# Kernel optimization log

Measured on AMD Instinct MI355X. Metric: run time of the kernel, lower is better.

The kernel has to match this reference:

```python
import jax, jax.numpy as jnp
import numpy as np

B, S, D, H, T_OUT = 256, 256, 64, 1024, 32  # batch, enc seq, input dim, hidden, decode steps


def setup_inputs() -> dict:
    key = jax.random.key(0)
    ks = jax.random.split(key, 15)
    p = lambda k, shape: jax.random.normal(k, shape, jnp.float32) * 0.05
    return {
        "X": jax.random.normal(ks[0], (B, S, D), jnp.float32),
        # encoder LSTM (2 layers); bias = b_ih + b_hh fused (same math)
        "enc_Wih0": p(ks[1], (4 * H, D)), "enc_Whh0": p(ks[2], (4 * H, H)), "enc_b0": p(ks[3], (4 * H,)),
        "enc_Wih1": p(ks[4], (4 * H, H)), "enc_Whh1": p(ks[5], (4 * H, H)), "enc_b1": p(ks[6], (4 * H,)),
        # decoder LSTM (2 layers, scalar input)
        "dec_Wih0": p(ks[7], (4 * H, 1)), "dec_Whh0": p(ks[8], (4 * H, H)), "dec_b0": p(ks[9], (4 * H,)),
        "dec_Wih1": p(ks[10], (4 * H, H)), "dec_Whh1": p(ks[11], (4 * H, H)), "dec_b1": p(ks[12], (4 * H,)),
        # output projection hidden -> 1
        "fc_W": p(ks[13], (1, H)), "fc_b": p(ks[14], (1,)),
    }


def _cell(x, h, c, Wih, Whh, b):
    # torch LSTM cell, gate order i, f, g, o
    gates = x @ Wih.T + h @ Whh.T + b  # [B, 4H]
    i, f, g, o = jnp.split(gates, 4, axis=-1)
    c = jax.nn.sigmoid(f) * c + jax.nn.sigmoid(i) * jnp.tanh(g)
    h = jax.nn.sigmoid(o) * jnp.tanh(c)
    return h, c


def reference(X, enc_Wih0, enc_Whh0, enc_b0, enc_Wih1, enc_Whh1, enc_b1,
              dec_Wih0, dec_Whh0, dec_b0, dec_Wih1, dec_Whh1, dec_b1,
              fc_W, fc_b):
    batch = X.shape[0]
    zeros = jnp.zeros((batch, H), X.dtype)

    def enc_layer(Wih, Whh, b, xs):  # xs: [S, B, Din]
        def step(carry, x_t):
            h, c = carry
            h, c = _cell(x_t, h, c, Wih, Whh, b)
            return (h, c), h
        (h, c), hs = jax.lax.scan(step, (zeros, zeros), xs)
        return hs, h, c

    xs = jnp.swapaxes(X, 0, 1)  # time-major [S, B, D]
    hs0, h0, c0 = enc_layer(enc_Wih0, enc_Whh0, enc_b0, xs)
    _, h1, c1 = enc_layer(enc_Wih1, enc_Whh1, enc_b1, hs0)

    inp0 = jnp.zeros((batch, 1), X.dtype)

    def dec_step(carry, _):
        dh0, dc0, dh1, dc1, inp = carry
        dh0, dc0 = _cell(inp, dh0, dc0, dec_Wih0, dec_Whh0, dec_b0)
        dh1, dc1 = _cell(dh0, dh1, dc1, dec_Wih1, dec_Whh1, dec_b1)
        pred = dh1 @ fc_W.T + fc_b  # [B, 1]; dropout is identity at inference
        return (dh0, dc0, dh1, dc1, pred), pred

    _, preds = jax.lax.scan(dec_step, (h0, c0, h1, c1, inp0), None, length=T_OUT)
    return jnp.transpose(preds, (1, 0, 2))  # [B, T_OUT, 1]
```

## Files before the change

### kernel.cpp

```cpp
#include <hip/hip_runtime.h>

#define B_ 256
#define S_ 256
#define D_ 64
#define H_ 1024
#define G4 4096
#define TOUT 32

typedef unsigned short u16;
typedef __attribute__((ext_vector_type(8))) short short8;
typedef __attribute__((ext_vector_type(4))) float float4v;

__device__ __forceinline__ float bf2f(u16 b) {
  return __uint_as_float(((unsigned int)b) << 16);
}
__device__ __forceinline__ u16 f2bf(float f) {
  unsigned int u = __float_as_uint(f);
  unsigned int r = (u + 0x7fffu + ((u >> 16) & 1u)) >> 16;
  return (u16)r;
}
__device__ __forceinline__ unsigned pack2(float a, float b) {
  return (unsigned)f2bf(a) | ((unsigned)f2bf(b) << 16);
}
__device__ __forceinline__ float sigm(float x) {
  return 1.f / (1.f + __expf(-x));
}
__device__ __forceinline__ float tanh_(float x) {
  float xc = fminf(fmaxf(x, -15.f), 15.f);
  float e = __expf(2.f * xc);
  return (e - 1.f) / (e + 1.f);
}

__global__ __launch_bounds__(256) void cvt_kernel(const float* __restrict__ src,
                                                  u16* __restrict__ dst, int n) {
  for (int i = blockIdx.x * blockDim.x + threadIdx.x; i < n;
       i += gridDim.x * blockDim.x)
    dst[i] = f2bf(src[i]);
}

__global__ __launch_bounds__(256) void zero_kernel(uint4* __restrict__ p, int n16) {
  for (int i = blockIdx.x * blockDim.x + threadIdx.x; i < n16;
       i += gridDim.x * blockDim.x)
    p[i] = make_uint4(0u, 0u, 0u, 0u);
}

struct LayerDesc {
  const u16* A0; int lda0;
  const u16* A1; int lda1; int klen0;
  const void* W0; int ldw0;
  const void* W1; int ldw1; int Ktot;
  const float* bias;
  const float* wcol;
  const float* inp;
  float* c;
  u16* h;
  int active;
};

template <bool WF32>
__global__ __launch_bounds__(256) void lstm_step_kernel(LayerDesc dA, LayerDesc dB)
{
  const bool second = (blockIdx.y >= 4);
  const LayerDesc d = second ? dB : dA;
  if (!d.active) return;

  __shared__ u16 As[2][64][72];
  __shared__ u16 Bs[2][64][72];
  __shared__ float Gs[64][68];

  const int tid = threadIdx.x;
  const int m0 = (second ? (blockIdx.y - 4) : blockIdx.y) * 64;
  const int n0 = blockIdx.x * 64;
  const int ub = n0 >> 2;
  const int r = tid >> 2;
  const int q = tid & 3;
  const int lane = tid & 63;
  const int wv = tid >> 6;
  const int wm = (wv >> 1) * 32;
  const int wn = (wv & 1) * 32;
  const int l16 = lane & 15;
  const int quad = lane >> 4;

  const int klen0 = d.klen0;
  const u16* aw0 = d.A0 + (size_t)(m0 + r) * d.lda0;
  const u16* aw1 = d.A1 + (size_t)(m0 + r) * d.lda1;
  const int orow = (r & 3) * H_ + ub + (r >> 2);
  const u16* bw0_h = (const u16*)d.W0 + (size_t)orow * d.ldw0;
  const u16* bw1_h = (const u16*)d.W1 + (size_t)orow * d.ldw1;
  const float* bw0_f = (const float*)d.W0 + (size_t)orow * d.ldw0;
  const float* bw1_f = (const float*)d.W1 + (size_t)orow * d.ldw1;

  uint4 av0, av1, bv0, bv1;
  float4 bf0, bf1, bf2, bf3;

  auto load_chunk = [&](int kc) {
    const int kg = kc * 64 + q * 16;
    const bool first = kg < klen0;
    const u16* pa = first ? (aw0 + kg) : (aw1 + (kg - klen0));
    av0 = *(const uint4*)pa;
    av1 = *(const uint4*)(pa + 8);
    if constexpr (WF32) {
      const float* pb = first ? (bw0_f + kg) : (bw1_f + (kg - klen0));
      bf0 = *(const float4*)pb;
      bf1 = *(const float4*)(pb + 4);
      bf2 = *(const float4*)(pb + 8);
      bf3 = *(const float4*)(pb + 12);
    } else {
      const u16* pb = first ? (bw0_h + kg) : (bw1_h + (kg - klen0));
      bv0 = *(const uint4*)pb;
      bv1 = *(const uint4*)(pb + 8);
    }
  };

  auto stage = [&](int buf) {
    if constexpr (WF32) {
      bv0 = make_uint4(pack2(bf0.x, bf0.y), pack2(bf0.z, bf0.w),
                       pack2(bf1.x, bf1.y), pack2(bf1.z, bf1.w));
      bv1 = make_uint4(pack2(bf2.x, bf2.y), pack2(bf2.z, bf2.w),
                       pack2(bf3.x, bf3.y), pack2(bf3.z, bf3.w));
    }
    *(uint4*)&As[buf][r][q * 16]     = av0;
    *(uint4*)&As[buf][r][q * 16 + 8] = av1;
    *(uint4*)&Bs[buf][r][q * 16]     = bv0;
    *(uint4*)&Bs[buf][r][q * 16 + 8] = bv1;
  };

  float4v acc00 = {}, acc01 = {}, acc10 = {}, acc11 = {};
  const int nch = d.Ktot >> 6;

  load_chunk(0);
  stage(0);
  if (nch > 1) load_chunk(1);
  __syncthreads();

  for (int kc = 0; kc < nch; ++kc) {
    const int cur = kc & 1;
#pragma unroll
    for (int ks = 0; ks < 2; ++ks) {
      const int kb = ks * 32 + quad * 8;
      short8 a0 = *(const short8*)&As[cur][wm + l16][kb];
      short8 a1 = *(const short8*)&As[cur][wm + 16 + l16][kb];
      short8 b0 = *(const short8*)&Bs[cur][wn + l16][kb];
      short8 b1 = *(const short8*)&Bs[cur][wn + 16 + l16][kb];
      acc00 = __builtin_amdgcn_mfma_f32_16x16x32_bf16(a0, b0, acc00, 0, 0, 0);
      acc01 = __builtin_amdgcn_mfma_f32_16x16x32_bf16(a0, b1, acc01, 0, 0, 0);
      acc10 = __builtin_amdgcn_mfma_f32_16x16x32_bf16(a1, b0, acc10, 0, 0, 0);
      acc11 = __builtin_amdgcn_mfma_f32_16x16x32_bf16(a1, b1, acc11, 0, 0, 0);
    }
    if (kc + 1 < nch) {
      stage(cur ^ 1);
      if (kc + 2 < nch) load_chunk(kc + 2);
      __syncthreads();
    }
  }

#pragma unroll
  for (int rr = 0; rr < 4; ++rr) {
    Gs[wm + quad * 4 + rr][wn + l16]           = acc00[rr];
    Gs[wm + quad * 4 + rr][wn + 16 + l16]      = acc01[rr];
    Gs[wm + 16 + quad * 4 + rr][wn + l16]      = acc10[rr];
    Gs[wm + 16 + quad * 4 + rr][wn + 16 + l16] = acc11[rr];
  }
  __syncthreads();

#pragma unroll
  for (int it = 0; it < 4; ++it) {
    const int p = tid + it * 256;
    const int bl = p >> 4;
    const int u = p & 15;
    const int J = ub + u;
    const int bg = m0 + bl;
    const float4v g = *(const float4v*)&Gs[bl][u * 4];
    float pi = g[0] + d.bias[J];
    float pf = g[1] + d.bias[H_ + J];
    float pg = g[2] + d.bias[2 * H_ + J];
    float po = g[3] + d.bias[3 * H_ + J];
    if (d.inp != nullptr) {
      const float iv = d.inp[bg];
      pi += iv * d.wcol[J];
      pf += iv * d.wcol[H_ + J];
      pg += iv * d.wcol[2 * H_ + J];
      po += iv * d.wcol[3 * H_ + J];
    }
    const size_t idx = (size_t)bg * H_ + J;
    const float c = d.c[idx];
    const float cn = sigm(pf) * c + sigm(pi) * tanh_(pg);
    d.c[idx] = cn;
    d.h[idx] = f2bf(sigm(po) * tanh_(cn));
  }
}

__global__ __launch_bounds__(256) void fc_kernel(
    const u16* __restrict__ h1, const float* __restrict__ fcW,
    const float* __restrict__ fcb, float* __restrict__ out,
    float* __restrict__ inp, int t)
{
  const int b = blockIdx.x;
  const int tid = threadIdx.x;
  const u16* hr = h1 + (size_t)b * H_ + tid * 4;
  const float* wr = fcW + tid * 4;
  float s = 0.f;
#pragma unroll
  for (int j = 0; j < 4; ++j) s += bf2f(hr[j]) * wr[j];
#pragma unroll
  for (int off = 32; off > 0; off >>= 1) s += __shfl_down(s, off, 64);
  __shared__ float red[4];
  if ((tid & 63) == 0) red[tid >> 6] = s;
  __syncthreads();
  if (tid == 0) {
    const float p = red[0] + red[1] + red[2] + red[3] + fcb[0];
    out[(size_t)b * TOUT + t] = p;
    inp[b] = p;
  }
}

extern "C" void kernel_launch(void* const* d_in, const int* in_sizes, int n_in,
                              void* d_out, int out_size, void* d_ws, size_t ws_size,
                              hipStream_t stream)
{
  const float* X     = (const float*)d_in[0];
  const float* eWih0 = (const float*)d_in[1];
  const float* eWhh0 = (const float*)d_in[2];
  const float* eb0   = (const float*)d_in[3];
  const float* eWih1 = (const float*)d_in[4];
  const float* eWhh1 = (const float*)d_in[5];
  const float* eb1   = (const float*)d_in[6];
  const float* dWih0 = (const float*)d_in[7];
  const float* dWhh0 = (const float*)d_in[8];
  const float* db0   = (const float*)d_in[9];
  const float* dWih1 = (const float*)d_in[10];
  const float* dWhh1 = (const float*)d_in[11];
  const float* db1   = (const float*)d_in[12];
  const float* fcW   = (const float*)d_in[13];
  const float* fcb   = (const float*)d_in[14];
  float* out = (float*)d_out;

  char* ws = (char*)d_ws;
  size_t off = 0;
  auto alloc = [&](size_t bytes) -> void* {
    void* p = ws + off;
    off += (bytes + 255) & ~(size_t)255;
    return p;
  };
  u16* h0buf[2], *h1buf[2];
  h0buf[0] = (u16*)alloc((size_t)B_ * H_ * 2);
  h0buf[1] = (u16*)alloc((size_t)B_ * H_ * 2);
  h1buf[0] = (u16*)alloc((size_t)B_ * H_ * 2);
  h1buf[1] = (u16*)alloc((size_t)B_ * H_ * 2);
  float* C0  = (float*)alloc((size_t)B_ * H_ * 4);
  float* C1  = (float*)alloc((size_t)B_ * H_ * 4);
  float* INP = (float*)alloc(B_ * 4);
  const size_t zbytes = off;
  u16* XB = (u16*)alloc((size_t)B_ * S_ * D_ * 2);
  u16* WB_eWih0 = (u16*)alloc((size_t)G4 * D_ * 2);
  u16* WB_eWhh0 = (u16*)alloc((size_t)G4 * H_ * 2);
  u16* WB_eWih1 = (u16*)alloc((size_t)G4 * H_ * 2);
  u16* WB_eWhh1 = (u16*)alloc((size_t)G4 * H_ * 2);
  u16* WB_dWhh0 = (u16*)alloc((size_t)G4 * H_ * 2);
  u16* WB_dWih1 = (u16*)alloc((size_t)G4 * H_ * 2);
  u16* WB_dWhh1 = (u16*)alloc((size_t)G4 * H_ * 2);
  const size_t need_full = off;
  const bool fast = (ws_size >= need_full);

  zero_kernel<<<dim3(256), dim3(256), 0, stream>>>((uint4*)ws, (int)(zbytes / 16));
  cvt_kernel<<<dim3(1024), dim3(256), 0, stream>>>(X, XB, B_ * S_ * D_);
  if (fast) {
    cvt_kernel<<<dim3(256), dim3(256), 0, stream>>>(eWih0, WB_eWih0, G4 * D_);
    cvt_kernel<<<dim3(1024), dim3(256), 0, stream>>>(eWhh0, WB_eWhh0, G4 * H_);
    cvt_kernel<<<dim3(1024), dim3(256), 0, stream>>>(eWih1, WB_eWih1, G4 * H_);
    cvt_kernel<<<dim3(1024), dim3(256), 0, stream>>>(eWhh1, WB_eWhh1, G4 * H_);
    cvt_kernel<<<dim3(1024), dim3(256), 0, stream>>>(dWhh0, WB_dWhh0, G4 * H_);
    cvt_kernel<<<dim3(1024), dim3(256), 0, stream>>>(dWih1, WB_dWih1, G4 * H_);
    cvt_kernel<<<dim3(1024), dim3(256), 0, stream>>>(dWhh1, WB_dWhh1, G4 * H_);
  }

  auto mk = [&](const u16* A0, int lda0, const u16* A1, int lda1, int klen0,
                const void* W0b, const void* W0f, int ldw0,
                const void* W1b, const void* W1f, int ldw1, int Ktot,
                const float* bias, const float* wcol, const float* inp,
                float* c, u16* h) {
    LayerDesc d;
    d.A0 = A0; d.lda0 = lda0; d.A1 = A1; d.lda1 = lda1; d.klen0 = klen0;
    d.W0 = fast ? W0b : W0f; d.ldw0 = ldw0;
    d.W1 = fast ? W1b : W1f; d.ldw1 = ldw1; d.Ktot = Ktot;
    d.bias = bias; d.wcol = wcol; d.inp = inp; d.c = c; d.h = h;
    d.active = 1;
    return d;
  };
  LayerDesc off_d = {};
  off_d.active = 0;

  auto launch = [&](dim3 grid, const LayerDesc& a, const LayerDesc& b) {
    if (fast)
      lstm_step_kernel<false><<<grid, dim3(256), 0, stream>>>(a, b);
    else
      lstm_step_kernel<true><<<grid, dim3(256), 0, stream>>>(a, b);
  };

  for (int u = 0; u <= S_; ++u) {
    LayerDesc d0 = off_d, d1 = off_d;
    if (u < S_) {
      const int t = u;
      d0 = mk(XB + t * D_, S_ * D_, h0buf[t & 1], H_, D_,
              WB_eWih0, eWih0, D_, WB_eWhh0, eWhh0, H_, 1088,
              eb0, nullptr, nullptr, C0, h0buf[(t + 1) & 1]);
    }
    if (u >= 1) {
      const int t = u - 1;
      d1 = mk(h0buf[(t + 1) & 1], H_, h1buf[t & 1], H_, H_,
              WB_eWih1, eWih1, H_, WB_eWhh1, eWhh1, H_, 2048,
              eb1, nullptr, nullptr, C1, h1buf[(t + 1) & 1]);
    }
    launch(dim3(64, 8), d0, d1);
  }

  for (int t = 0; t < TOUT; ++t) {
    u16* h0i = h0buf[t & 1]; u16* h0o = h0buf[(t + 1) & 1];
    u16* h1i = h1buf[t & 1]; u16* h1o = h1buf[(t + 1) & 1];
    LayerDesc dl0 = mk(h0i, H_, h0i, H_, 1024,
                       WB_dWhh0, dWhh0, H_, WB_dWhh0, dWhh0, H_, 1024,
                       db0, dWih0, INP, C0, h0o);
    launch(dim3(64, 4), dl0, off_d);
    LayerDesc dl1 = mk(h0o, H_, h1i, H_, H_,
                       WB_dWih1, dWih1, H_, WB_dWhh1, dWhh1, H_, 2048,
                       db1, nullptr, nullptr, C1, h1o);
    launch(dim3(64, 4), dl1, off_d);
    fc_kernel<<<dim3(B_), dim3(256), 0, stream>>>(h1o, fcW, fcb, out, INP, t);
  }
}
```

Baseline: 6.183 ms.

## Overlap decoder layer-1 step with next layer-0 recurrent GEMM, fuse FC projection

Restructures the decoder so the layer-0 recurrent GEMM for step t+1 (which depends only on h0) runs in the same launch as the layer-1 step t. Raw gate pre-activations go to a global buffer, and a separate cell kernel applies the input-dependent term once the prediction is known. The FC projection is fused into the layer-1 epilogue through shuffle reduction and atomics, which removes the per-step fc kernel. This adds a large gate buffer round trip and atomic accumulation in exchange for fewer serial launches and better GPU fill.

```diff
diff --git a/kernel.cpp b/kernel.cpp
--- a/kernel.cpp
+++ b/kernel.cpp
@@ -55,6 +55,9 @@
   float* c;
   u16* h;
   int active;
+  float* gout;
+  const float* fcW;
+  float* pred;
 };
 
 template <bool WF32>
@@ -162,6 +165,21 @@
     Gs[wm + 16 + quad * 4 + rr][wn + 16 + l16] = acc11[rr];
   }
   __syncthreads();
+
+  if (d.gout != nullptr) {
+#pragma unroll
+    for (int it = 0; it < 4; ++it) {
+      const int p = tid + it * 256;
+      const int bl = p >> 4;
+      const int u = p & 15;
+      const int J = ub + u;
+      const int bg = m0 + bl;
+      const float4v g = *(const float4v*)&Gs[bl][u * 4];
+      *(float4*)&d.gout[((size_t)bg * H_ + J) * 4] =
+          make_float4(g[0], g[1], g[2], g[3]);
+    }
+    return;
+  }
 
 #pragma unroll
   for (int it = 0; it < 4; ++it) {
@@ -186,8 +204,52 @@
     const float c = d.c[idx];
     const float cn = sigm(pf) * c + sigm(pi) * tanh_(pg);
     d.c[idx] = cn;
-    d.h[idx] = f2bf(sigm(po) * tanh_(cn));
-  }
+    const float hv = sigm(po) * tanh_(cn);
+    d.h[idx] = f2bf(hv);
+    if (d.pred != nullptr) {
+      float s = hv * d.fcW[J];
+      s += __shfl_xor(s, 1, 64);
+      s += __shfl_xor(s, 2, 64);
+      s += __shfl_xor(s, 4, 64);
+      s += __shfl_xor(s, 8, 64);
+      if (u == 0) atomicAdd(&d.pred[bg], s);
+    }
+  }
+}
+
+__global__ __launch_bounds__(256) void dec_cell_kernel(
+    const float* __restrict__ GBUF, const float* __restrict__ bias,
+    const float* __restrict__ wcol, const float* __restrict__ pred_prev,
+    const float* __restrict__ fcb, float* __restrict__ C,
+    u16* __restrict__ hout)
+{
+  const int b = blockIdx.x;
+  const int tid = threadIdx.x;
+  const float iv = (pred_prev != nullptr) ? (pred_prev[b] + fcb[0]) : 0.f;
+#pragma unroll
+  for (int k = 0; k < 4; ++k) {
+    const int J = tid + k * 256;
+    const float4 g = *(const float4*)&GBUF[((size_t)b * H_ + J) * 4];
+    const float pi = g.x + bias[J]          + iv * wcol[J];
+    const float pf = g.y + bias[H_ + J]     + iv * wcol[H_ + J];
+    const float pg = g.z + bias[2 * H_ + J] + iv * wcol[2 * H_ + J];
+    const float po = g.w + bias[3 * H_ + J] + iv * wcol[3 * H_ + J];
+    const size_t idx = (size_t)b * H_ + J;
+    const float c0 = C[idx];
+    const float cn = sigm(pf) * c0 + sigm(pi) * tanh_(pg);
+    C[idx] = cn;
+    hout[idx] = f2bf(sigm(po) * tanh_(cn));
+  }
+}
+
+__global__ __launch_bounds__(256) void dec_out_kernel(
+    const float* __restrict__ PRED, const float* __restrict__ fcb,
+    float* __restrict__ out)
+{
+  const int gid = blockIdx.x * 256 + threadIdx.x;
+  const int b = gid >> 5;
+  const int t = gid & 31;
+  out[gid] = PRED[t * B_ + b] + fcb[0];
 }
 
 __global__ __launch_bounds__(256) void fc_kernel(
@@ -247,9 +309,10 @@
   h0buf[1] = (u16*)alloc((size_t)B_ * H_ * 2);
   h1buf[0] = (u16*)alloc((size_t)B_ * H_ * 2);
   h1buf[1] = (u16*)alloc((size_t)B_ * H_ * 2);
-  float* C0  = (float*)alloc((size_t)B_ * H_ * 4);
-  float* C1  = (float*)alloc((size_t)B_ * H_ * 4);
-  float* INP = (float*)alloc(B_ * 4);
+  float* C0   = (float*)alloc((size_t)B_ * H_ * 4);
+  float* C1   = (float*)alloc((size_t)B_ * H_ * 4);
+  float* INP  = (float*)alloc(B_ * 4);
+  float* PRED = (float*)alloc((size_t)TOUT * B_ * 4);
   const size_t zbytes = off;
   u16* XB = (u16*)alloc((size_t)B_ * S_ * D_ * 2);
   u16* WB_eWih0 = (u16*)alloc((size_t)G4 * D_ * 2);
@@ -259,6 +322,7 @@
   u16* WB_dWhh0 = (u16*)alloc((size_t)G4 * H_ * 2);
   u16* WB_dWih1 = (u16*)alloc((size_t)G4 * H_ * 2);
   u16* WB_dWhh1 = (u16*)alloc((size_t)G4 * H_ * 2);
+  float* GBUF   = (float*)alloc((size_t)B_ * H_ * 4 * 4);
   const size_t need_full = off;
   const bool fast = (ws_size >= need_full);
 
@@ -285,6 +349,7 @@
     d.W1 = fast ? W1b : W1f; d.ldw1 = ldw1; d.Ktot = Ktot;
     d.bias = bias; d.wcol = wcol; d.inp = inp; d.c = c; d.h = h;
     d.active = 1;
+    d.gout = nullptr; d.fcW = nullptr; d.pred = nullptr;
     return d;
   };
   LayerDesc off_d = {};
@@ -312,6 +377,38 @@
               eb1, nullptr, nullptr, C1, h1buf[(t + 1) & 1]);
     }
     launch(dim3(64, 8), d0, d1);
+  }
+
+  if (fast) {
+    LayerDesc g0 = mk(h0buf[0], H_, h0buf[0], H_, 1024,
+                      WB_dWhh0, dWhh0, H_, WB_dWhh0, dWhh0, H_, 1024,
+                      db0, nullptr, nullptr, C0, nullptr);
+    g0.gout = GBUF;
+    launch(dim3(64, 4), g0, off_d);
+    dec_cell_kernel<<<dim3(B_), dim3(256), 0, stream>>>(
+        GBUF, db0, dWih0, nullptr, fcb, C0, h0buf[1]);
+
+    for (int t = 0; t < TOUT; ++t) {
+      LayerDesc dA = mk(h0buf[(t + 1) & 1], H_, h1buf[t & 1], H_, 1024,
+                        WB_dWih1, dWih1, H_, WB_dWhh1, dWhh1, H_, 2048,
+                        db1, nullptr, nullptr, C1, h1buf[(t + 1) & 1]);
+      dA.fcW = fcW;
+      dA.pred = PRED + (size_t)t * B_;
+      LayerDesc dB = off_d;
+      const bool more = (t + 1 < TOUT);
+      if (more) {
+        dB = mk(h0buf[(t + 1) & 1], H_, h0buf[(t + 1) & 1], H_, 1024,
+                WB_dWhh0, dWhh0, H_, WB_dWhh0, dWhh0, H_, 1024,
+                db0, nullptr, nullptr, C0, nullptr);
+        dB.gout = GBUF;
+      }
+      launch(dim3(64, more ? 8 : 4), dA, dB);
+      if (more)
+        dec_cell_kernel<<<dim3(B_), dim3(256), 0, stream>>>(
+            GBUF, db0, dWih0, PRED + (size_t)t * B_, fcb, C0, h0buf[t & 1]);
+    }
+    dec_out_kernel<<<dim3(TOUT), dim3(256), 0, stream>>>(PRED, fcb, out);
+    return;
   }
 
   for (int t = 0; t < TOUT; ++t) {
```

Measured after the change: 6.142 ms. About the same (-0.7%).
